# Optimization experiments

Measured on AMD Instinct MI355X. Metric: run time of the kernel, lower is better.

Reference implementation:

```python
import jax, jax.numpy as jnp
import numpy as np

B, N, D = 2, 2048, 1536
HEADS, KVH, DQK, DV = 8, 1, 128, 192
G = HEADS // KVH  # query groups per kv head
NP, DP = 512, 128  # pairwise seq len (coarse), pairwise feature dim
SCALE = DQK ** -0.5
CLAMP = 5.0
MOMENTUM = 0.1  # BatchRMSNorm: 1 - 0.9
EPS = 1e-5


def layernorm(x, w, b):
    mu = jnp.mean(x, axis=-1, keepdims=True)
    var = jnp.mean(jnp.square(x - mu), axis=-1, keepdims=True)
    return (x - mu) * jax.lax.rsqrt(var + EPS) * w + b


def setup_inputs() -> dict:
    key = jax.random.key(0)
    ks = jax.random.split(key, 6)
    w = lambda k, shape: jax.random.normal(k, shape, jnp.float32) * 0.02
    return {
        "x": jax.random.normal(ks[0], (B, N, D), jnp.float32),
        "pairwise": jax.random.normal(ks[1], (B, NP, NP, DP), jnp.float32),
        "w_qkv": w(ks[2], (D, HEADS * DQK + KVH * DQK + KVH * DV)),
        "q_w": jnp.ones((DQK,), jnp.float32), "q_b": jnp.zeros((DQK,), jnp.float32),
        "k_w": jnp.ones((DQK,), jnp.float32), "k_b": jnp.zeros((DQK,), jnp.float32),
        "v_w": jnp.ones((DV,), jnp.float32), "v_b": jnp.zeros((DV,), jnp.float32),
        "bias_gamma": jnp.ones((DP,), jnp.float32),
        "bias_beta": jnp.zeros((DP,), jnp.float32),
        "bias_running_var": jnp.ones((DP,), jnp.float32),
        "w_bias": w(ks[3], (DP, HEADS)),
        "w_out": w(ks[4], (HEADS * DV, D)),
        "b_out": jnp.zeros((D,), jnp.float32),
    }


def reference(x, pairwise, w_qkv, q_w, q_b, k_w, k_b, v_w, v_b,
              bias_gamma, bias_beta, bias_running_var, w_bias, w_out, b_out):
    b, n, _ = x.shape
    qkv = x @ w_qkv
    q, k, v = jnp.split(qkv, [HEADS * DQK, HEADS * DQK + KVH * DQK], axis=-1)
    # split heads: q -> b g h n d, k/v -> b h n d
    q = q.reshape(b, n, G, KVH, DQK).transpose(0, 2, 3, 1, 4)
    k = k.reshape(b, n, KVH, DQK).transpose(0, 2, 1, 3)
    v = v.reshape(b, n, KVH, DV).transpose(0, 2, 1, 3)
    q = layernorm(q, q_w, q_b)
    k = layernorm(k, k_w, k_b)
    v = layernorm(v, v_w, v_b)

    sim = jnp.einsum('bghid,bhjd->bghij', q, k) * SCALE

    # BatchRMSNorm (training update of running_var, then normalize)
    flat = pairwise.reshape(-1, DP)
    batch_var = jnp.var(flat, axis=0)  # unbiased=False
    rv = bias_running_var * (1.0 - MOMENTUM) + MOMENTUM * batch_var
    std = jnp.sqrt(rv + EPS)
    normed = pairwise / std * bias_gamma + bias_beta
    bias = jax.nn.gelu(normed, approximate=False) @ w_bias  # b i j (g h)
    bias = bias.reshape(b, NP, NP, G, KVH).transpose(0, 3, 4, 1, 2)  # b g h i j
    r = n // NP  # expand_factor
    bias = jnp.repeat(jnp.repeat(bias, r, axis=-2), r, axis=-1)

    sim = jnp.tanh((sim + bias) / CLAMP) * CLAMP  # softclamp
    attn = jax.nn.softmax(sim, axis=-1)
    out = jnp.einsum('bghij,bhjd->bghid', attn, v)
    out = out.transpose(0, 3, 1, 2, 4).reshape(b, n, HEADS * DV)  # merge heads
    return out @ w_out + b_out
```

## Files before the change

kernel.cpp:

```cpp
#include <hip/hip_runtime.h>
#include <math.h>

typedef _Float16 f16;
typedef unsigned int u32;
typedef __attribute__((ext_vector_type(8))) f16 f16x8;
typedef __attribute__((ext_vector_type(4))) f16 f16x4;
typedef __attribute__((ext_vector_type(4))) float f32x4;
typedef __attribute__((ext_vector_type(16))) float f32x16;

#define DEV static __device__ __forceinline__

#define SEQ 2048
#define DMODEL 1536
#define NHEADS 8
#define DQK 128
#define DVV 192
#define QKVW 1344
#define SCALEQK 0.08838834764831845f
#define LOG2E 1.4426950408889634f

#define OFF_WQKVT 0ull
#define OFF_WOUTT 4128768ull
#define OFF_XH    8847360ull
#define OFF_QKV   21430272ull
#define OFF_Q     43450368ull
#define OFF_K     51838976ull
#define OFF_V     52887552ull
#define OFF_VT    54460416ull
#define OFF_PART  56033280ull
#define OFF_SG    57081856ull
#define OFF_BIASC 57082880ull
#define OFF_AO    65471488ull
#define OFF_OP    78054400ull
#define OFF_LS    128386048ull

DEV float fexp2(float x){
#if __has_builtin(__builtin_amdgcn_exp2f)
  return __builtin_amdgcn_exp2f(x);
#else
  return exp2f(x);
#endif
}
DEV float frcp(float x){
#if __has_builtin(__builtin_amdgcn_rcpf)
  return __builtin_amdgcn_rcpf(x);
#else
  return 1.0f/x;
#endif
}

typedef u32 __attribute__((address_space(1))) u32g;
typedef u32 __attribute__((address_space(3))) u32l;
DEV void g2l16(const void* g, void* l){
  __builtin_amdgcn_global_load_lds((const u32g*)g, (u32l*)l, 16, 0, 0);
}

#define MFMA32(a,b,c) __builtin_amdgcn_mfma_f32_32x32x16_f16(a,b,c,0,0,0)
#define MFMA16(a,b,c) __builtin_amdgcn_mfma_f32_16x16x32_f16(a,b,c,0,0,0)

DEV f32x16 zero16(){
  f32x16 v;
  #pragma unroll
  for (int i=0;i<16;i++) v[i]=0.f;
  return v;
}
DEV f32x4 zero4(){
  f32x4 v;
  #pragma unroll
  for (int i=0;i<4;i++) v[i]=0.f;
  return v;
}

DEV float gelu_f(float x){
  float z  = 0.70710678118654752440f * x;
  float az = fabsf(z);
  float t  = frcp(1.f + 0.3275911f*az);
  float poly = t*(0.254829592f + t*(-0.284496736f + t*(1.421413741f +
               t*(-1.453152027f + t*1.061405429f))));
  float e  = 1.f - poly*fexp2(-z*z*LOG2E);
  float er = (z < 0.f) ? -e : e;
  return 0.5f*x*(1.f + er);
}

__global__ __launch_bounds__(256) void k1_prep(const float* __restrict__ wq, f16* __restrict__ wqT,
                                               const float* __restrict__ wo, f16* __restrict__ woT,
                                               const float* __restrict__ X, f16* __restrict__ Xh){
  __shared__ float t[32][33];
  int bid = blockIdx.x, tid = threadIdx.x;
  if (bid >= 4320){
    size_t i0 = (size_t)(bid - 4320)*2048 + (size_t)tid*8;
    f32x4 a = *(const f32x4*)(X + i0);
    f32x4 b = *(const f32x4*)(X + i0 + 4);
    f16x8 o;
    #pragma unroll
    for (int e=0;e<4;e++){ o[e] = (f16)a[e]; o[4+e] = (f16)b[e]; }
    *(f16x8*)(Xh + i0) = o;
    return;
  }
  int tx = tid & 31, ty = tid >> 5;
  const float* src; f16* dst; int N, x, y;
  if (bid < 2016){ src = wq; dst = wqT; N = 1344; x = bid % 48; y = bid / 48; }
  else { int b2 = bid - 2016; src = wo; dst = woT; N = 1536; x = b2 % 48; y = b2 / 48; }
  int k0 = x*32, n0 = y*32;
  #pragma unroll
  for (int i=0;i<4;i++){ int r = ty+8*i; t[r][tx] = src[(size_t)(k0+r)*N + n0+tx]; }
  __syncthreads();
  #pragma unroll
  for (int i=0;i<4;i++){ int r = ty+8*i; dst[(size_t)(n0+r)*1536 + k0+tx] = (f16)t[tx][r]; }
}

DEV void gemm256_body(const f16* __restrict__ A, const f16* __restrict__ WT,
                      float* __restrict__ C, int ldc, const float* __restrict__ bo,
                      char* lds, int bx, int by, int tid){
  int nb = bx*64, mb = by*256;
  int w = tid>>6, lane = tid&63, li = lane&31, h = lane>>5;
  int srow = lane>>3, sc = lane&7;
  f32x16 acc[2][2];
  acc[0][0]=zero16(); acc[0][1]=zero16(); acc[1][0]=zero16(); acc[1][1]=zero16();

#define G_STAGE(buf, kt_) do { \
    char* ad = lds + (buf)*40960; \
    _Pragma("unroll") \
    for (int s=0;s<8;s++){ \
      int slot = w*8+s; int mlr = slot*8 + srow; int cs = sc ^ (srow&7); \
      g2l16(A + (size_t)(mb+mlr)*DMODEL + (kt_)*64 + cs*8, ad + slot*1024); \
    } \
    char* bd = lds + (buf)*40960 + 32768; \
    _Pragma("unroll") \
    for (int s=0;s<2;s++){ \
      int slot = w*2+s; int nl = slot*8 + srow; int cs = sc ^ (srow&7); \
      g2l16(WT + (size_t)(nb+nl)*DMODEL + (kt_)*64 + cs*8, bd + slot*1024); \
    } } while(0)

  G_STAGE(0,0);
  __syncthreads();
  for (int kt=0; kt<24; kt++){
    int cur = kt&1;
    if (kt<23) G_STAGE(cur^1, kt+1);
    const char* ad = lds + cur*40960;
    const char* bd = lds + cur*40960 + 32768;
    #pragma unroll
    for (int ks=0; ks<4; ks++){
      int cso = ((2*ks+h) ^ (li&7))*16;
      f16x8 a0 = *(const f16x8*)(ad + (w*64      + li)*128 + cso);
      f16x8 a1 = *(const f16x8*)(ad + (w*64 + 32 + li)*128 + cso);
      f16x8 b0 = *(const f16x8*)(bd + (           li)*128 + cso);
      f16x8 b1 = *(const f16x8*)(bd + (      32 + li)*128 + cso);
      acc[0][0] = MFMA32(a0, b0, acc[0][0]);
      acc[0][1] = MFMA32(a0, b1, acc[0][1]);
      acc[1][0] = MFMA32(a1, b0, acc[1][0]);
      acc[1][1] = MFMA32(a1, b1, acc[1][1]);
    }
    __syncthreads();
  }
  float bo0 = bo ? bo[nb+li] : 0.f, bo1 = bo ? bo[nb+32+li] : 0.f;
  #pragma unroll
  for (int mi=0; mi<2; mi++)
    #pragma unroll
    for (int nf=0; nf<2; nf++)
      #pragma unroll
      for (int r=0;r<16;r++){
        int m = mb + w*64 + mi*32 + (r&3) + 8*(r>>2) + 4*h;
        int n = nb + nf*32 + li;
        C[(size_t)m*ldc + n] = acc[mi][nf][r] + (nf ? bo1 : bo0);
      }
#undef G_STAGE
}

DEV void pvar_body(const float* __restrict__ pw, float* __restrict__ partials,
                   char* smem, int id, int tid){
  int q = tid & 31, rg = tid >> 5;
  f32x4 s1 = zero4(), s2 = zero4();
  const float* p0 = pw + ((size_t)id*512 + rg)*128 + q*4;
  #pragma unroll 4
  for (int it=0; it<64; it++){
    f32x4 v = *(const f32x4*)(p0 + (size_t)it*1024);
    s1 += v; s2 += v*v;
  }
  f32x4* r1 = (f32x4*)smem; f32x4* r2 = r1 + 256;
  r1[tid] = s1; r2[tid] = s2;
  __syncthreads();
  if (tid < 64){
    int qq = tid & 31;
    f32x4* rr = (tid >= 32) ? r2 : r1;
    f32x4 a = rr[qq];
    #pragma unroll
    for (int g=1; g<8; g++) a += rr[g*32+qq];
    *(f32x4*)(partials + (size_t)id*256 + ((tid>=32)?128:0) + qq*4) = a;
  }
}

__global__ __launch_bounds__(256,2) void k2_qkv_pvar(const f16* __restrict__ Xh,
    const f16* __restrict__ WT, float* __restrict__ qkv,
    const float* __restrict__ pw, float* __restrict__ partials){
  __shared__ char smem[81920];
  int bid = blockIdx.x, tid = threadIdx.x;
  if (bid % 5 == 0){
    int qid = bid/5;
    int l = (qid&7)*42 + (qid>>3);
    gemm256_body(Xh, WT, qkv, QKVW, (const float*)0, smem, l%21, l/21, tid);
  } else {
    int pid = bid - bid/5 - 1;
    if (pid < 1024) pvar_body(pw, partials, smem, pid, tid);
  }
}

DEV void ln_unit(const float* __restrict__ qkv,
    const float* __restrict__ qw, const float* __restrict__ qb,
    const float* __restrict__ kw, const float* __restrict__ kb,
    const float* __restrict__ vw, const float* __restrict__ vb,
    f16* __restrict__ Q, f16* __restrict__ K, f16* __restrict__ V,
    int unit, int lane){
  int row = unit / 10, seg = unit - row*10;
  int b = row >> 11, n = row & 2047;
  const float* base = qkv + (size_t)row*QKVW;
  if (seg < 9){
    int off = seg*128;
    float x0 = base[off+lane], x1 = base[off+64+lane];
    float s = x0+x1;
    #pragma unroll
    for (int d=32; d>=1; d>>=1) s += __shfl_xor(s, d);
    float mu = s*(1.f/128.f);
    float d0 = x0-mu, d1 = x1-mu;
    float vv = d0*d0 + d1*d1;
    #pragma unroll
    for (int d=32; d>=1; d>>=1) vv += __shfl_xor(vv, d);
    float istd = rsqrtf(vv*(1.f/128.f) + 1e-5f);
    const float* W  = (seg<8)? qw : kw;
    const float* Bi = (seg<8)? qb : kb;
    f16* dst = (seg<8) ? (Q + ((size_t)(b*NHEADS+seg)*SEQ + n)*DQK)
                       : (K + ((size_t)(b*SEQ+n))*DQK);
    dst[lane]    = (f16)(d0*istd*W[lane] + Bi[lane]);
    dst[lane+64] = (f16)(d1*istd*W[lane+64] + Bi[lane+64]);
  } else {
    float x0 = base[1152+lane], x1 = base[1152+64+lane], x2 = base[1152+128+lane];
    float s = x0+x1+x2;
    #pragma unroll
    for (int d=32; d>=1; d>>=1) s += __shfl_xor(s, d);
    float mu = s*(1.f/192.f);
    float d0=x0-mu, d1=x1-mu, d2=x2-mu;
    float vv = d0*d0+d1*d1+d2*d2;
    #pragma unroll
    for (int d=32; d>=1; d>>=1) vv += __shfl_xor(vv, d);
    float istd = rsqrtf(vv*(1.f/192.f) + 1e-5f);
    f16* dst = V + (size_t)(b*SEQ+n)*DVV;
    dst[lane]     = (f16)(d0*istd*vw[lane] + vb[lane]);
    dst[lane+64]  = (f16)(d1*istd*vw[lane+64] + vb[lane+64]);
    dst[lane+128] = (f16)(d2*istd*vw[lane+128] + vb[lane+128]);
  }
}

__global__ __launch_bounds__(256,4) void k3_ln_finvar(const float* __restrict__ qkv,
    const float* __restrict__ qw, const float* __restrict__ qb,
    const float* __restrict__ kw, const float* __restrict__ kb,
    const float* __restrict__ vw, const float* __restrict__ vb,
    f16* __restrict__ Q, f16* __restrict__ K, f16* __restrict__ V,
    const float* __restrict__ partials, const float* __restrict__ rvar,
    const float* __restrict__ gamma, const float* __restrict__ beta,
    float* __restrict__ sg, float* __restrict__ sb){
  __shared__ float sh[256];
  int bid = blockIdx.x, tid = threadIdx.x;
  if (bid < 10240){
    ln_unit(qkv, qw,qb,kw,kb,vw,vb, Q,K,V, bid*4 + (tid>>6), tid&63);
  } else {
    int c = tid & 127, wh = tid >> 7;
    float acc = 0.f;
    #pragma unroll 8
    for (int i=0;i<1024;i++) acc += partials[i*256 + wh*128 + c];
    sh[tid] = acc;
    __syncthreads();
    if (tid < 128){
      float s1 = sh[tid], s2 = sh[tid+128];
      const float Minv = 1.f/524288.f;
      float m = s1*Minv;
      float var = s2*Minv - m*m;
      float rv = rvar[tid]*0.9f + 0.1f*var;
      sg[tid] = rsqrtf(rv + 1e-5f)*gamma[tid];
      sb[tid] = beta[tid];
    }
  }
}

DEV void bias_body(const float* __restrict__ pw,
    const float* __restrict__ sg, const float* __restrict__ sb,
    const float* __restrict__ wb, f16* __restrict__ biasc, int bias_id, int tid){
  int w = tid>>6, lane = tid&63;
  int il = lane&15, kg = lane>>4;
  f16x8 bw[4];
  float sgr[32], sbr[32];
  #pragma unroll
  for (int t=0;t<4;t++)
    #pragma unroll
    for (int e=0;e<8;e++){
      int k = t*32 + kg*8 + e;
      bw[t][e] = (f16)((il<8) ? wb[k*8 + il] : 0.f);
      sgr[t*8+e] = sg[k];
      sbr[t*8+e] = sb[k];
    }
  for (int it=0; it<8; it++){
    int tile = bias_id*4 + w + it*4096;
    size_t rg = (size_t)tile*16 + il;
    f32x4 acc = zero4();
    #pragma unroll
    for (int t=0;t<4;t++){
      const float* sp = pw + rg*128 + t*32 + kg*8;
      f32x4 v0 = *(const f32x4*)sp;
      f32x4 v1 = *(const f32x4*)(sp+4);
      f16x8 af;
      #pragma unroll
      for (int e=0;e<4;e++) af[e]   = (f16)gelu_f(v0[e]*sgr[t*8+e]   + sbr[t*8+e]);
      #pragma unroll
      for (int e=0;e<4;e++) af[4+e] = (f16)gelu_f(v1[e]*sgr[t*8+4+e] + sbr[t*8+4+e]);
      acc = MFMA16(af, bw[t], acc);
    }
    if (il < 8){
      #pragma unroll
      for (int r=0;r<4;r++){
        size_t rr = (size_t)tile*16 + kg*4 + r;
        int bb = (int)(rr >> 18);
        int rem = (int)(rr & 262143);
        int ii = rem >> 9, jj = rem & 511;
        biasc[(((size_t)(bb*8 + il)*512) + ii)*512 + jj] = (f16)acc[r];
      }
    }
  }
}

DEV void vtrans_body(const f16* __restrict__ V, f16* __restrict__ VT,
                     f16 (*t)[33], int id, int tid){
  int b = id / 384, rem = id - b*384;
  int d0 = (rem % 6)*32, j0 = (rem / 6)*32;
  int tx = tid & 31, ty = tid >> 5;
  #pragma unroll
  for (int i=0;i<4;i++){ int r = ty+8*i; t[r][tx] = V[((size_t)b*SEQ + j0+r)*DVV + d0+tx]; }
  __syncthreads();
  #pragma unroll
  for (int i=0;i<4;i++){ int r = ty+8*i; VT[((size_t)b*DVV + d0+r)*SEQ + j0+tx] = t[tx][r]; }
}

__global__ __launch_bounds__(256,2) void k4_bias_vtrans(const float* __restrict__ pw,
    const float* __restrict__ sg, const float* __restrict__ sb,
    const float* __restrict__ wb, f16* __restrict__ biasc,
    const f16* __restrict__ V, f16* __restrict__ VT){
  __shared__ f16 tt[32][33];
  int bid = blockIdx.x, tid = threadIdx.x;
  if (bid < 1536){
    if (bid & 1) bias_body(pw, sg, sb, wb, biasc, bid>>1, tid);
    else         vtrans_body(V, VT, tt, bid>>1, tid);
  } else {
    bias_body(pw, sg, sb, wb, biasc, 768 + (bid - 1536), tid);
  }
}

__global__ __launch_bounds__(256,2) void attn(const f16* __restrict__ Q, const f16* __restrict__ K,
                                              const f16* __restrict__ VT, const f16* __restrict__ biasc,
                                              float* __restrict__ Opart, float* __restrict__ Ls){
  __shared__ char lds[81920];
  int bid = blockIdx.x;
  int half = bid & 1, bgqt = bid >> 1;
  int bg = bgqt & 15, qt = bgqt >> 4;
  int b = bg >> 3;
  int tid = threadIdx.x;
  int w = tid >> 6, lane = tid & 63;
  int li = lane & 31, h = lane >> 5;

  const f16* Qb = Q  + (size_t)bg*SEQ*DQK;
  const f16* Kb = K  + (size_t)b*SEQ*DQK;
  const f16* Vb = VT + (size_t)b*DVV*SEQ;

  int qrow = qt*128 + w*32 + li;
  f16x8 qf[8];
  #pragma unroll
  for (int ks=0; ks<8; ks++)
    qf[ks] = *(const f16x8*)(Qb + (size_t)qrow*DQK + ks*16 + h*8);

  const f16* brow = biasc + ((size_t)bg*512 + (qrow>>2))*512;

  f32x16 oacc[6];
  #pragma unroll
  for (int nf=0;nf<6;nf++) oacc[nf] = zero16();
  float lsum = 0.f;

  int kl_row = lane >> 4, kl_c = lane & 15;
  int vl_row = lane >> 3, vl_c = lane & 7;

#define STAGE(buf, jt_) do { \
    char* kd = lds + (buf)*40960; \
    const f16* ksrc = Kb + (size_t)(jt_)*64*DQK; \
    _Pragma("unroll") \
    for (int s=0;s<4;s++){ \
      int slot = w*4+s; int jr = slot*4 + kl_row; int cs = kl_c ^ (jr&7); \
      g2l16(ksrc + (size_t)jr*DQK + cs*8, kd + slot*1024); \
    } \
    char* vd = lds + (buf)*40960 + 16384; \
    _Pragma("unroll") \
    for (int s=0;s<6;s++){ \
      int slot = w*6+s; int dvr = slot*8 + vl_row; int cs = vl_c ^ (dvr&7); \
      g2l16(Vb + (size_t)dvr*SEQ + (size_t)(jt_)*64 + cs*8, vd + slot*1024); \
    } } while(0)

  int jt0 = half*16;
  STAGE(0, jt0);

  const float CS = SCALEQK * (2.f*LOG2E/5.f);
  const float CB = 2.f*LOG2E/5.f;
  const float CP = 5.f*LOG2E;

  for (int jj=0; jj<16; jj++){
    int jt = jt0 + jj;
    int cur = jj & 1;
    __syncthreads();
    if (jj < 15) STAGE(cur^1, jt+1);
    const char* kb_ = lds + cur*40960;
    const char* vb_ = lds + cur*40960 + 16384;

    f32x16 s0 = zero16(), s1 = zero16();
    #pragma unroll
    for (int ks=0; ks<8; ks++){
      int cso = ((2*ks + h) ^ (li&7))*16;
      f16x8 kf0 = *(const f16x8*)(kb_ + (     li)*256 + cso);
      f16x8 kf1 = *(const f16x8*)(kb_ + (32 + li)*256 + cso);
      s0 = MFMA32(kf0, qf[ks], s0);
      s1 = MFMA32(kf1, qf[ks], s1);
    }

    f16x8 pa[2][2];
    #pragma unroll
    for (int sub=0; sub<2; sub++){
      const f32x16& sacc = sub ? s1 : s0;
      int jb4 = jt*16 + sub*8;
      f16x8 bv = *(const f16x8*)(brow + jb4);
      float bt[4];
      #pragma unroll
      for (int q=0;q<4;q++){
        float b0 = (float)bv[2*q], b1 = (float)bv[2*q+1];
        bt[q] = (h ? b1 : b0) * CB;
      }
      float p[16], xp[16];
      #pragma unroll
      for (int r=0;r<16;r++){
        float u2 = sacc[r]*CS + bt[r>>2];
        float E  = fexp2(u2);
        float tn = 1.f - 2.f*frcp(E + 1.f);
        float pr = fexp2(tn * CP);
        p[r] = pr;
        lsum += pr;
      }
      #pragma unroll
      for (int r=0;r<16;r++) xp[r] = __shfl_xor(p[r], 32);
      #pragma unroll
      for (int ks2=0; ks2<2; ks2++){
        #pragma unroll
        for (int e=0;e<4;e++) pa[sub][ks2][e] = (f16)(h ? xp[8*ks2+4+e] : p[8*ks2+e]);
        #pragma unroll
        for (int e=4;e<8;e++) pa[sub][ks2][e] = (f16)(h ? p[8*ks2+e]    : xp[8*ks2+e-4]);
      }
    }
    #pragma unroll
    for (int sub=0; sub<2; sub++)
      #pragma unroll
      for (int ks2=0; ks2<2; ks2++)
        #pragma unroll
        for (int nf=0; nf<6; nf++){
          int dvr = nf*32 + li;
          int cj = (sub*4 + 2*ks2 + h) ^ (dvr&7);
          f16x8 vf = *(const f16x8*)(vb_ + dvr*128 + cj*16);
          oacc[nf] = MFMA32(pa[sub][ks2], vf, oacc[nf]);
        }
  }
  float* Ob = Opart + (size_t)(bgqt*2 + half)*128*192;
  #pragma unroll
  for (int nf=0; nf<6; nf++)
    #pragma unroll
    for (int r=0;r<16;r++){
      int il = (r&3) + 8*(r>>2) + 4*h;
      Ob[(size_t)(w*32 + il)*192 + nf*32 + li] = oacc[nf][r];
    }
  float ltot = lsum + __shfl_xor(lsum, 32);
  if (h == 0) Ls[(size_t)(bgqt*2 + half)*128 + w*32 + li] = ltot;
#undef STAGE
}

__global__ __launch_bounds__(256) void attn_combine(const float* __restrict__ Opart,
                                                    const float* __restrict__ Ls,
                                                    f16* __restrict__ AO){
  int tid = threadIdx.x;
  int pr = blockIdx.x*16 + (tid>>4);
  int sub = tid & 15;
  int bgqt = pr >> 7, row = pr & 127;
  int bg = bgqt & 15, qt = bgqt >> 4;
  int b = bg >> 3, g = bg & 7;
  int n = qt*128 + row;
  float l0 = Ls[(size_t)(bgqt*2 + 0)*128 + row];
  float l1 = Ls[(size_t)(bgqt*2 + 1)*128 + row];
  float linv = 1.f / (l0 + l1);
  const float* O0 = Opart + ((size_t)(bgqt*2 + 0)*128 + row)*192 + sub*12;
  const float* O1 = Opart + ((size_t)(bgqt*2 + 1)*128 + row)*192 + sub*12;
  f16* dst = AO + ((size_t)(b*SEQ + n)*NHEADS + g)*DVV + sub*12;
  #pragma unroll
  for (int j=0;j<3;j++){
    f32x4 a = *(const f32x4*)(O0 + 4*j);
    f32x4 c = *(const f32x4*)(O1 + 4*j);
    f16x4 o;
    #pragma unroll
    for (int e=0;e<4;e++) o[e] = (f16)((a[e] + c[e]) * linv);
    *(f16x4*)(dst + 4*j) = o;
  }
}

__global__ __launch_bounds__(256,2) void out_gemm(const f16* __restrict__ A, const f16* __restrict__ WT,
                                                  const float* __restrict__ bo, float* __restrict__ out){
  __shared__ char lds[81920];
  int bid = blockIdx.x, tid = threadIdx.x;
  int l = (bid&7)*48 + (bid>>3);
  gemm256_body(A, WT, out, DMODEL, bo, lds, l%24, l/24, tid);
}

extern "C" void kernel_launch(void* const* d_in, const int* in_sizes, int n_in,
                              void* d_out, int out_size, void* d_ws, size_t ws_size,
                              hipStream_t stream) {
  (void)in_sizes; (void)n_in; (void)out_size; (void)ws_size;
  const float* x        = (const float*)d_in[0];
  const float* pairwise = (const float*)d_in[1];
  const float* w_qkv    = (const float*)d_in[2];
  const float* q_w      = (const float*)d_in[3];
  const float* q_b      = (const float*)d_in[4];
  const float* k_w      = (const float*)d_in[5];
  const float* k_b      = (const float*)d_in[6];
  const float* v_w      = (const float*)d_in[7];
  const float* v_b      = (const float*)d_in[8];
  const float* bgamma   = (const float*)d_in[9];
  const float* bbeta    = (const float*)d_in[10];
  const float* brvar    = (const float*)d_in[11];
  const float* w_bias   = (const float*)d_in[12];
  const float* w_out    = (const float*)d_in[13];
  const float* b_out    = (const float*)d_in[14];
  float* out = (float*)d_out;

  char* ws = (char*)d_ws;
  f16*   wqkvT = (f16*)(ws + OFF_WQKVT);
  f16*   woutT = (f16*)(ws + OFF_WOUTT);
  f16*   Xh    = (f16*)(ws + OFF_XH);
  float* qkvb  = (float*)(ws + OFF_QKV);
  f16*   Qh    = (f16*)(ws + OFF_Q);
  f16*   Kh    = (f16*)(ws + OFF_K);
  f16*   Vh    = (f16*)(ws + OFF_V);
  f16*   VTh   = (f16*)(ws + OFF_VT);
  float* part  = (float*)(ws + OFF_PART);
  float* sg    = (float*)(ws + OFF_SG);
  float* sb    = sg + 128;
  f16*   biasc = (f16*)(ws + OFF_BIASC);
  f16*   AOh   = (f16*)(ws + OFF_AO);
  float* Opart = (float*)(ws + OFF_OP);
  float* Lsw   = (float*)(ws + OFF_LS);

  k1_prep<<<7392, 256, 0, stream>>>(w_qkv, wqkvT, w_out, woutT, x, Xh);
  k2_qkv_pvar<<<1680, 256, 0, stream>>>(Xh, wqkvT, qkvb, pairwise, part);
  k3_ln_finvar<<<10241, 256, 0, stream>>>(qkvb, q_w,q_b,k_w,k_b,v_w,v_b, Qh, Kh, Vh,
                                          part, brvar, bgamma, bbeta, sg, sb);
  k4_bias_vtrans<<<1792, 256, 0, stream>>>(pairwise, sg, sb, w_bias, biasc, Vh, VTh);
  attn<<<512, 256, 0, stream>>>(Qh, Kh, VTh, biasc, Opart, Lsw);
  attn_combine<<<2048, 256, 0, stream>>>(Opart, Lsw, AOh);
  out_gemm<<<384, 256, 0, stream>>>(AOh, woutT, b_out, out);
}
```

Measured before the change: 337.6 us.

## Fuse Q/K/V layernorm into QKV GEMM epilogue, drop fp32 qkv buffer

The QKV projection GEMM is restructured so that each block computes a 128-row by full-head-width tile (128 for Q/K heads, 192 for V). Per-row layernorm is then done in registers with cross-lane shuffles and written straight to the f16 Q/K/V layouts. This removes the fp32 qkv intermediate, which was about 22 MB written and then read back, along with the separate layernorm pass. The variance finalisation moves to its own single-block kernel. The cost is a narrower M tile with a wider N tile, which changes MFMA reuse and register pressure in the GEMM, and the GEMM has 320 tiles instead of 336.

Result: no change. 334.9 us (-0.8%).

```diff
diff --git a/kernel.cpp b/kernel.cpp
--- a/kernel.cpp
+++ b/kernel.cpp
@@ -22,17 +22,16 @@
 #define OFF_WQKVT 0ull
 #define OFF_WOUTT 4128768ull
 #define OFF_XH    8847360ull
-#define OFF_QKV   21430272ull
-#define OFF_Q     43450368ull
-#define OFF_K     51838976ull
-#define OFF_V     52887552ull
-#define OFF_VT    54460416ull
-#define OFF_PART  56033280ull
-#define OFF_SG    57081856ull
-#define OFF_BIASC 57082880ull
-#define OFF_AO    65471488ull
-#define OFF_OP    78054400ull
-#define OFF_LS    128386048ull
+#define OFF_Q     21430272ull
+#define OFF_K     29818880ull
+#define OFF_V     30867456ull
+#define OFF_VT    32440320ull
+#define OFF_PART  34013184ull
+#define OFF_SG    35061760ull
+#define OFF_BIASC 35062784ull
+#define OFF_AO    43451392ull
+#define OFF_OP    56034304ull
+#define OFF_LS    106365952ull
 
 DEV float fexp2(float x){
 #if __has_builtin(__builtin_amdgcn_exp2f)
@@ -109,62 +108,80 @@
   for (int i=0;i<4;i++){ int r = ty+8*i; dst[(size_t)(n0+r)*1536 + k0+tx] = (f16)t[tx][r]; }
 }
 
-DEV void gemm256_body(const f16* __restrict__ A, const f16* __restrict__ WT,
-                      float* __restrict__ C, int ldc, const float* __restrict__ bo,
-                      char* lds, int bx, int by, int tid){
-  int nb = bx*64, mb = by*256;
+template<int NF>
+DEV void qkvln_body(const f16* __restrict__ A, const f16* __restrict__ WT, int nbase,
+                    const float* __restrict__ lnw, const float* __restrict__ lnb,
+                    f16* __restrict__ d0, size_t bstride,
+                    char* lds, int mt, int tid){
+  const int BN = NF*32;
+  int mb = mt*128;
   int w = tid>>6, lane = tid&63, li = lane&31, h = lane>>5;
   int srow = lane>>3, sc = lane&7;
-  f32x16 acc[2][2];
-  acc[0][0]=zero16(); acc[0][1]=zero16(); acc[1][0]=zero16(); acc[1][1]=zero16();
-
-#define G_STAGE(buf, kt_) do { \
+  f32x16 acc[NF];
+  #pragma unroll
+  for (int nf=0;nf<NF;nf++) acc[nf] = zero16();
+
+#define QL_STAGE(buf, kt_) do { \
     char* ad = lds + (buf)*40960; \
     _Pragma("unroll") \
-    for (int s=0;s<8;s++){ \
-      int slot = w*8+s; int mlr = slot*8 + srow; int cs = sc ^ (srow&7); \
-      g2l16(A + (size_t)(mb+mlr)*DMODEL + (kt_)*64 + cs*8, ad + slot*1024); \
+    for (int s=0;s<4;s++){ \
+      int slot = w*4+s; int row = slot*8 + srow; int cs = sc ^ (srow&7); \
+      g2l16(A + (size_t)(mb+row)*DMODEL + (kt_)*64 + cs*8, ad + slot*1024); \
     } \
-    char* bd = lds + (buf)*40960 + 32768; \
+    char* bd = lds + (buf)*40960 + 16384; \
     _Pragma("unroll") \
-    for (int s=0;s<2;s++){ \
-      int slot = w*2+s; int nl = slot*8 + srow; int cs = sc ^ (srow&7); \
-      g2l16(WT + (size_t)(nb+nl)*DMODEL + (kt_)*64 + cs*8, bd + slot*1024); \
+    for (int s=0;s<NF;s++){ \
+      int slot = w*NF+s; int row = slot*8 + srow; int cs = sc ^ (srow&7); \
+      g2l16(WT + (size_t)(nbase+row)*DMODEL + (kt_)*64 + cs*8, bd + slot*1024); \
     } } while(0)
 
-  G_STAGE(0,0);
+  QL_STAGE(0,0);
   __syncthreads();
   for (int kt=0; kt<24; kt++){
     int cur = kt&1;
-    if (kt<23) G_STAGE(cur^1, kt+1);
+    if (kt<23) QL_STAGE(cur^1, kt+1);
     const char* ad = lds + cur*40960;
-    const char* bd = lds + cur*40960 + 32768;
+    const char* bd = lds + cur*40960 + 16384;
     #pragma unroll
     for (int ks=0; ks<4; ks++){
       int cso = ((2*ks+h) ^ (li&7))*16;
-      f16x8 a0 = *(const f16x8*)(ad + (w*64      + li)*128 + cso);
-      f16x8 a1 = *(const f16x8*)(ad + (w*64 + 32 + li)*128 + cso);
-      f16x8 b0 = *(const f16x8*)(bd + (           li)*128 + cso);
-      f16x8 b1 = *(const f16x8*)(bd + (      32 + li)*128 + cso);
-      acc[0][0] = MFMA32(a0, b0, acc[0][0]);
-      acc[0][1] = MFMA32(a0, b1, acc[0][1]);
-      acc[1][0] = MFMA32(a1, b0, acc[1][0]);
-      acc[1][1] = MFMA32(a1, b1, acc[1][1]);
+      f16x8 af = *(const f16x8*)(ad + (w*32 + li)*128 + cso);
+      #pragma unroll
+      for (int nf=0; nf<NF; nf++){
+        f16x8 bf = *(const f16x8*)(bd + (nf*32 + li)*128 + cso);
+        acc[nf] = MFMA32(af, bf, acc[nf]);
+      }
     }
     __syncthreads();
   }
-  float bo0 = bo ? bo[nb+li] : 0.f, bo1 = bo ? bo[nb+32+li] : 0.f;
-  #pragma unroll
-  for (int mi=0; mi<2; mi++)
-    #pragma unroll
-    for (int nf=0; nf<2; nf++)
-      #pragma unroll
-      for (int r=0;r<16;r++){
-        int m = mb + w*64 + mi*32 + (r&3) + 8*(r>>2) + 4*h;
-        int n = nb + nf*32 + li;
-        C[(size_t)m*ldc + n] = acc[mi][nf][r] + (nf ? bo1 : bo0);
-      }
-#undef G_STAGE
+
+  float Wc[NF], Bc[NF];
+  #pragma unroll
+  for (int nf=0;nf<NF;nf++){ Wc[nf] = lnw[nf*32+li]; Bc[nf] = lnb[nf*32+li]; }
+  const float invBN = 1.f/(float)BN;
+  #pragma unroll
+  for (int rr=0; rr<16; rr++){
+    float s = 0.f;
+    #pragma unroll
+    for (int nf=0;nf<NF;nf++) s += acc[nf][rr];
+    #pragma unroll
+    for (int d=16; d>=1; d>>=1) s += __shfl_xor(s, d);
+    float mu = s*invBN;
+    float vv = 0.f;
+    #pragma unroll
+    for (int nf=0;nf<NF;nf++){ float dd = acc[nf][rr]-mu; vv += dd*dd; }
+    #pragma unroll
+    for (int d=16; d>=1; d>>=1) vv += __shfl_xor(vv, d);
+    float istd = rsqrtf(vv*invBN + 1e-5f);
+    int r = (rr&3) + 8*(rr>>2) + 4*h;
+    int m = mb + w*32 + r;
+    int bb = m >> 11, nseq = m & 2047;
+    f16* drow = d0 + (size_t)bb*bstride + (size_t)nseq*BN;
+    #pragma unroll
+    for (int nf=0;nf<NF;nf++)
+      drow[nf*32+li] = (f16)((acc[nf][rr]-mu)*istd*Wc[nf] + Bc[nf]);
+  }
+#undef QL_STAGE
 }
 
 DEV void pvar_body(const float* __restrict__ pw, float* __restrict__ partials,
@@ -190,94 +207,52 @@
   }
 }
 
-__global__ __launch_bounds__(256,2) void k2_qkv_pvar(const f16* __restrict__ Xh,
-    const f16* __restrict__ WT, float* __restrict__ qkv,
+__global__ __launch_bounds__(256,2) void k2_qkvln_pvar(const f16* __restrict__ Xh,
+    const f16* __restrict__ WT,
+    const float* __restrict__ qw, const float* __restrict__ qb,
+    const float* __restrict__ kw, const float* __restrict__ kb,
+    const float* __restrict__ vw, const float* __restrict__ vb,
+    f16* __restrict__ Q, f16* __restrict__ K, f16* __restrict__ V,
     const float* __restrict__ pw, float* __restrict__ partials){
   __shared__ char smem[81920];
   int bid = blockIdx.x, tid = threadIdx.x;
   if (bid % 5 == 0){
     int qid = bid/5;
-    int l = (qid&7)*42 + (qid>>3);
-    gemm256_body(Xh, WT, qkv, QKVW, (const float*)0, smem, l%21, l/21, tid);
+    if (qid >= 320) return;
+    int l = (qid&7)*40 + (qid>>3);
+    int seg = l >> 5, mt = l & 31;
+    if (seg < 8)
+      qkvln_body<4>(Xh, WT, seg*128, qw, qb, Q + (size_t)seg*SEQ*DQK,
+                    (size_t)NHEADS*SEQ*DQK, smem, mt, tid);
+    else if (seg == 8)
+      qkvln_body<4>(Xh, WT, 1024, kw, kb, K, (size_t)SEQ*DQK, smem, mt, tid);
+    else
+      qkvln_body<6>(Xh, WT, 1152, vw, vb, V, (size_t)SEQ*DVV, smem, mt, tid);
   } else {
     int pid = bid - bid/5 - 1;
     if (pid < 1024) pvar_body(pw, partials, smem, pid, tid);
   }
 }
 
-DEV void ln_unit(const float* __restrict__ qkv,
-    const float* __restrict__ qw, const float* __restrict__ qb,
-    const float* __restrict__ kw, const float* __restrict__ kb,
-    const float* __restrict__ vw, const float* __restrict__ vb,
-    f16* __restrict__ Q, f16* __restrict__ K, f16* __restrict__ V,
-    int unit, int lane){
-  int row = unit / 10, seg = unit - row*10;
-  int b = row >> 11, n = row & 2047;
-  const float* base = qkv + (size_t)row*QKVW;
-  if (seg < 9){
-    int off = seg*128;
-    float x0 = base[off+lane], x1 = base[off+64+lane];
-    float s = x0+x1;
-    #pragma unroll
-    for (int d=32; d>=1; d>>=1) s += __shfl_xor(s, d);
-    float mu = s*(1.f/128.f);
-    float d0 = x0-mu, d1 = x1-mu;
-    float vv = d0*d0 + d1*d1;
-    #pragma unroll
-    for (int d=32; d>=1; d>>=1) vv += __shfl_xor(vv, d);
-    float istd = rsqrtf(vv*(1.f/128.f) + 1e-5f);
-    const float* W  = (seg<8)? qw : kw;
-    const float* Bi = (seg<8)? qb : kb;
-    f16* dst = (seg<8) ? (Q + ((size_t)(b*NHEADS+seg)*SEQ + n)*DQK)
-                       : (K + ((size_t)(b*SEQ+n))*DQK);
-    dst[lane]    = (f16)(d0*istd*W[lane] + Bi[lane]);
-    dst[lane+64] = (f16)(d1*istd*W[lane+64] + Bi[lane+64]);
-  } else {
-    float x0 = base[1152+lane], x1 = base[1152+64+lane], x2 = base[1152+128+lane];
-    float s = x0+x1+x2;
-    #pragma unroll
-    for (int d=32; d>=1; d>>=1) s += __shfl_xor(s, d);
-    float mu = s*(1.f/192.f);
-    float d0=x0-mu, d1=x1-mu, d2=x2-mu;
-    float vv = d0*d0+d1*d1+d2*d2;
-    #pragma unroll
-    for (int d=32; d>=1; d>>=1) vv += __shfl_xor(vv, d);
-    float istd = rsqrtf(vv*(1.f/192.f) + 1e-5f);
-    f16* dst = V + (size_t)(b*SEQ+n)*DVV;
-    dst[lane]     = (f16)(d0*istd*vw[lane] + vb[lane]);
-    dst[lane+64]  = (f16)(d1*istd*vw[lane+64] + vb[lane+64]);
-    dst[lane+128] = (f16)(d2*istd*vw[lane+128] + vb[lane+128]);
-  }
-}
-
-__global__ __launch_bounds__(256,4) void k3_ln_finvar(const float* __restrict__ qkv,
-    const float* __restrict__ qw, const float* __restrict__ qb,
-    const float* __restrict__ kw, const float* __restrict__ kb,
-    const float* __restrict__ vw, const float* __restrict__ vb,
-    f16* __restrict__ Q, f16* __restrict__ K, f16* __restrict__ V,
-    const float* __restrict__ partials, const float* __restrict__ rvar,
-    const float* __restrict__ gamma, const float* __restrict__ beta,
-    float* __restrict__ sg, float* __restrict__ sb){
+__global__ __launch_bounds__(256) void finvar_k(const float* __restrict__ partials,
+    const float* __restrict__ rvar, const float* __restrict__ gamma,
+    const float* __restrict__ beta, float* __restrict__ sg, float* __restrict__ sb){
   __shared__ float sh[256];
-  int bid = blockIdx.x, tid = threadIdx.x;
-  if (bid < 10240){
-    ln_unit(qkv, qw,qb,kw,kb,vw,vb, Q,K,V, bid*4 + (tid>>6), tid&63);
-  } else {
-    int c = tid & 127, wh = tid >> 7;
-    float acc = 0.f;
-    #pragma unroll 8
-    for (int i=0;i<1024;i++) acc += partials[i*256 + wh*128 + c];
-    sh[tid] = acc;
-    __syncthreads();
-    if (tid < 128){
-      float s1 = sh[tid], s2 = sh[tid+128];
-      const float Minv = 1.f/524288.f;
-      float m = s1*Minv;
-      float var = s2*Minv - m*m;
-      float rv = rvar[tid]*0.9f + 0.1f*var;
-      sg[tid] = rsqrtf(rv + 1e-5f)*gamma[tid];
-      sb[tid] = beta[tid];
-    }
+  int tid = threadIdx.x;
+  int c = tid & 127, wh = tid >> 7;
+  float acc = 0.f;
+  #pragma unroll 8
+  for (int i=0;i<1024;i++) acc += partials[i*256 + wh*128 + c];
+  sh[tid] = acc;
+  __syncthreads();
+  if (tid < 128){
+    float s1 = sh[tid], s2 = sh[tid+128];
+    const float Minv = 1.f/524288.f;
+    float m = s1*Minv;
+    float var = s2*Minv - m*m;
+    float rv = rvar[tid]*0.9f + 0.1f*var;
+    sg[tid] = rsqrtf(rv + 1e-5f)*gamma[tid];
+    sb[tid] = beta[tid];
   }
 }
 
@@ -506,6 +481,64 @@
     for (int e=0;e<4;e++) o[e] = (f16)((a[e] + c[e]) * linv);
     *(f16x4*)(dst + 4*j) = o;
   }
+}
+
+DEV void gemm256_body(const f16* __restrict__ A, const f16* __restrict__ WT,
+                      float* __restrict__ C, int ldc, const float* __restrict__ bo,
+                      char* lds, int bx, int by, int tid){
+  int nb = bx*64, mb = by*256;
+  int w = tid>>6, lane = tid&63, li = lane&31, h = lane>>5;
+  int srow = lane>>3, sc = lane&7;
+  f32x16 acc[2][2];
+  acc[0][0]=zero16(); acc[0][1]=zero16(); acc[1][0]=zero16(); acc[1][1]=zero16();
+
+#define G_STAGE(buf, kt_) do { \
+    char* ad = lds + (buf)*40960; \
+    _Pragma("unroll") \
+    for (int s=0;s<8;s++){ \
+      int slot = w*8+s; int mlr = slot*8 + srow; int cs = sc ^ (srow&7); \
+      g2l16(A + (size_t)(mb+mlr)*DMODEL + (kt_)*64 + cs*8, ad + slot*1024); \
+    } \
+    char* bd = lds + (buf)*40960 + 32768; \
+    _Pragma("unroll") \
+    for (int s=0;s<2;s++){ \
+      int slot = w*2+s; int nl = slot*8 + srow; int cs = sc ^ (srow&7); \
+      g2l16(WT + (size_t)(nb+nl)*DMODEL + (kt_)*64 + cs*8, bd + slot*1024); \
+    } } while(0)
+
+  G_STAGE(0,0);
+  __syncthreads();
+  for (int kt=0; kt<24; kt++){
+    int cur = kt&1;
+    if (kt<23) G_STAGE(cur^1, kt+1);
+    const char* ad = lds + cur*40960;
+    const char* bd = lds + cur*40960 + 32768;
+    #pragma unroll
+    for (int ks=0; ks<4; ks++){
+      int cso = ((2*ks+h) ^ (li&7))*16;
+      f16x8 a0 = *(const f16x8*)(ad + (w*64      + li)*128 + cso);
+      f16x8 a1 = *(const f16x8*)(ad + (w*64 + 32 + li)*128 + cso);
+      f16x8 b0 = *(const f16x8*)(bd + (           li)*128 + cso);
+      f16x8 b1 = *(const f16x8*)(bd + (      32 + li)*128 + cso);
+      acc[0][0] = MFMA32(a0, b0, acc[0][0]);
+      acc[0][1] = MFMA32(a0, b1, acc[0][1]);
+      acc[1][0] = MFMA32(a1, b0, acc[1][0]);
+      acc[1][1] = MFMA32(a1, b1, acc[1][1]);
+    }
+    __syncthreads();
+  }
+  float bo0 = bo ? bo[nb+li] : 0.f, bo1 = bo ? bo[nb+32+li] : 0.f;
+  #pragma unroll
+  for (int mi=0; mi<2; mi++)
+    #pragma unroll
+    for (int nf=0; nf<2; nf++)
+      #pragma unroll
+      for (int r=0;r<16;r++){
+        int m = mb + w*64 + mi*32 + (r&3) + 8*(r>>2) + 4*h;
+        int n = nb + nf*32 + li;
+        C[(size_t)m*ldc + n] = acc[mi][nf][r] + (nf ? bo1 : bo0);
+      }
+#undef G_STAGE
 }
 
 __global__ __launch_bounds__(256,2) void out_gemm(const f16* __restrict__ A, const f16* __restrict__ WT,
@@ -541,7 +574,6 @@
   f16*   wqkvT = (f16*)(ws + OFF_WQKVT);
   f16*   woutT = (f16*)(ws + OFF_WOUTT);
   f16*   Xh    = (f16*)(ws + OFF_XH);
-  float* qkvb  = (float*)(ws + OFF_QKV);
   f16*   Qh    = (f16*)(ws + OFF_Q);
   f16*   Kh    = (f16*)(ws + OFF_K);
   f16*   Vh    = (f16*)(ws + OFF_V);
@@ -555,9 +587,9 @@
   float* Lsw   = (float*)(ws + OFF_LS);
 
   k1_prep<<<7392, 256, 0, stream>>>(w_qkv, wqkvT, w_out, woutT, x, Xh);
-  k2_qkv_pvar<<<1680, 256, 0, stream>>>(Xh, wqkvT, qkvb, pairwise, part);
-  k3_ln_finvar<<<10241, 256, 0, stream>>>(qkvb, q_w,q_b,k_w,k_b,v_w,v_b, Qh, Kh, Vh,
-                                          part, brvar, bgamma, bbeta, sg, sb);
+  k2_qkvln_pvar<<<1680, 256, 0, stream>>>(Xh, wqkvT, q_w,q_b,k_w,k_b,v_w,v_b,
+                                          Qh, Kh, Vh, pairwise, part);
+  finvar_k<<<1, 256, 0, stream>>>(part, brvar, bgamma, bbeta, sg, sb);
   k4_bias_vtrans<<<1792, 256, 0, stream>>>(pairwise, sg, sb, w_bias, biasc, Vh, VTh);
   attn<<<512, 256, 0, stream>>>(Qh, Kh, VTh, biasc, Opart, Lsw);
   attn_combine<<<2048, 256, 0, stream>>>(Opart, Lsw, AOh);
```
